# Optimization experiments

Measured on AMD Instinct MI355X. Metric: run time of the kernel, lower is better.

The kernel has to match this reference:

```python
import jax, jax.numpy as jnp
import numpy as np

N = 50000
E = 800000
IN_DIM = 128
HID = 32
HEADS = 4
OUT_DIM = 64
NEG_SLOPE = 0.2


def gat_layer(x, src, dst, W, al, ar, b, heads, dout):
    # x: [N, din]; W: [din, heads*dout]; al/ar: [heads, dout]; b: [heads*dout]
    n = x.shape[0]
    feat = (x @ W).reshape(n, heads, dout)              # [N, H, D]
    el = jnp.sum(feat * al, axis=-1)                    # [N, H] attention (src side)
    er = jnp.sum(feat * ar, axis=-1)                    # [N, H] attention (dst side)
    e = jax.nn.leaky_relu(el[src] + er[dst], NEG_SLOPE)  # [E, H]
    # segment softmax over incoming edges of each destination node
    m = jax.ops.segment_max(e, dst, num_segments=n)     # [N, H]
    ex = jnp.exp(e - m[dst])                            # [E, H]
    s = jax.ops.segment_sum(ex, dst, num_segments=n)    # [N, H]
    alpha = ex / s[dst]                                 # [E, H]
    msg = alpha[:, :, None] * feat[src]                 # [E, H, D]
    out = jax.ops.segment_sum(msg, dst, num_segments=n)  # [N, H, D]
    return out + b.reshape(1, heads, dout)


def setup_inputs() -> dict:
    key = jax.random.key(0)
    ks = jax.random.split(key, 16)
    h = jax.random.normal(ks[0], (N, IN_DIM), dtype=jnp.float32)
    src = jax.random.randint(ks[1], (E,), 0, N, dtype=jnp.int32)
    dst = jax.random.randint(ks[2], (E,), 0, N, dtype=jnp.int32)

    def glorot(k, shape):
        fan = shape[0] + shape[-1]
        return jax.random.normal(k, shape, dtype=jnp.float32) * np.sqrt(2.0 / fan)

    W1 = glorot(ks[3], (IN_DIM, HEADS * HID))
    al1 = glorot(ks[4], (HEADS, HID))
    ar1 = glorot(ks[5], (HEADS, HID))
    b1 = jnp.zeros((HEADS * HID,), dtype=jnp.float32)
    W2 = glorot(ks[6], (HEADS * HID, HEADS * HID))
    al2 = glorot(ks[7], (HEADS, HID))
    ar2 = glorot(ks[8], (HEADS, HID))
    b2 = jnp.zeros((HEADS * HID,), dtype=jnp.float32)
    W3 = glorot(ks[9], (HEADS * HID, OUT_DIM))
    al3 = glorot(ks[10], (1, OUT_DIM))
    ar3 = glorot(ks[11], (1, OUT_DIM))
    b3 = jnp.zeros((OUT_DIM,), dtype=jnp.float32)
    return {"h": h, "src": src, "dst": dst,
            "W1": W1, "al1": al1, "ar1": ar1, "b1": b1,
            "W2": W2, "al2": al2, "ar2": ar2, "b2": b2,
            "W3": W3, "al3": al3, "ar3": ar3, "b3": b3}


def reference(h, src, dst, W1, al1, ar1, b1, W2, al2, ar2, b2, W3, al3, ar3, b3):
    # dropout layers are identity in eval mode
    x = gat_layer(h, src, dst, W1, al1, ar1, b1, HEADS, HID).reshape(N, -1)
    x = jax.nn.elu(x)
    x = gat_layer(x, src, dst, W2, al2, ar2, b2, HEADS, HID).reshape(N, -1)
    x = jax.nn.elu(x)
    x = gat_layer(x, src, dst, W3, al3, ar3, b3, 1, OUT_DIM).mean(axis=1)
    return x
```

## Files before the change

kernel.cpp:

```cpp
#include <hip/hip_runtime.h>
#include <hip/hip_bf16.h>
#include <math.h>

#define NNODES 50000
#define NEDGES 800000

static inline int cdiv(int a, int b) { return (a + b - 1) / b; }


__global__ void zero_deg(int* __restrict__ deg) {
    int i = blockIdx.x * blockDim.x + threadIdx.x;
    if (i < NNODES) deg[i] = 0;
}

__global__ void count_deg(const int* __restrict__ dst, int* __restrict__ deg) {
    int e = blockIdx.x * blockDim.x + threadIdx.x;
    if (e < NEDGES) atomicAdd(&deg[dst[e]], 1);
}

__global__ void scan_rowptr(const int* __restrict__ deg, int* __restrict__ rowptr,
                            int* __restrict__ cursor) {
    __shared__ int wsum[16];
    __shared__ int wpre[16];
    const int tid = threadIdx.x;
    const int lane = tid & 63, wid = tid >> 6;
    int carry = 0;
    const int ntiles = (NNODES + 4095) / 4096;
    for (int t = 0; t < ntiles; t++) {
        int i0 = t * 4096 + tid * 4;
        int4 v = make_int4(0, 0, 0, 0);
        if (i0 < NNODES) v = *(const int4*)&deg[i0];
        int lsum = v.x + v.y + v.z + v.w;
        int x = lsum;
#pragma unroll
        for (int off = 1; off < 64; off <<= 1) {
            int y = __shfl_up(x, off);
            if (lane >= off) x += y;
        }
        if (lane == 63) wsum[wid] = x;
        __syncthreads();
        if (wid == 0) {
            int w = (lane < 16) ? wsum[lane] : 0;
            int xs = w;
#pragma unroll
            for (int off = 1; off < 16; off <<= 1) {
                int y = __shfl_up(xs, off);
                if (lane >= off) xs += y;
            }
            if (lane < 16) wpre[lane] = xs - w;
        }
        __syncthreads();
        int excl = carry + wpre[wid] + x - lsum;
        if (i0 < NNODES) {
            int4 r;
            r.x = excl; r.y = r.x + v.x; r.z = r.y + v.y; r.w = r.z + v.z;
            *(int4*)&rowptr[i0] = r;
            *(int4*)&cursor[i0] = r;
        }
        carry += wpre[15] + wsum[15];
        __syncthreads();
    }
    if (tid == 0) rowptr[NNODES] = carry;
}

__global__ void scatter_src(const int* __restrict__ src, const int* __restrict__ dst,
                            int* __restrict__ cursor, int* __restrict__ csr_src) {
    int e = blockIdx.x * blockDim.x + threadIdx.x;
    if (e < NEDGES) {
        int pos = atomicAdd(&cursor[dst[e]], 1);
        csr_src[pos] = src[e];
    }
}

template <int DIN, int DOUT, int H, int NB>
__global__ void gemm_attn(const float* __restrict__ x, const float* __restrict__ W,
                          const float* __restrict__ al, const float* __restrict__ ar,
                          __hip_bfloat16* __restrict__ feat, float* __restrict__ el,
                          float* __restrict__ er) {
    constexpr int D = DOUT / H;
    __shared__ float xs[NB * DIN];
    const int node0 = blockIdx.x * NB;
    const int d = threadIdx.x;

    const float4* xg = (const float4*)&x[node0 * DIN];
    float4* xs4 = (float4*)xs;
    for (int idx = d; idx < NB * DIN / 4; idx += DOUT) xs4[idx] = xg[idx];
    __syncthreads();

    float accv[NB];
#pragma unroll
    for (int nb = 0; nb < NB; nb++) accv[nb] = 0.f;

    for (int k = 0; k < DIN; k++) {
        float w = W[k * DOUT + d];
#pragma unroll
        for (int nb = 0; nb < NB; nb++) accv[nb] += xs[nb * DIN + k] * w;
    }

    const float alv = al[d], arv = ar[d];
    const int h = d / D;
#pragma unroll
    for (int nb = 0; nb < NB; nb++) {
        float a = accv[nb];
        feat[(node0 + nb) * DOUT + d] = __float2bfloat16(a);
        float pl = a * alv, pr = a * arv;
#pragma unroll
        for (int off = D / 2; off > 0; off >>= 1) {
            pl += __shfl_xor(pl, off);
            pr += __shfl_xor(pr, off);
        }
        if ((d & (D - 1)) == 0) {
            el[(node0 + nb) * H + h] = pl;
            er[(node0 + nb) * H + h] = pr;
        }
    }
}

template <int DOUT, int H>
__global__ void node_aggregate(const int* __restrict__ rowptr, const int* __restrict__ csr_src,
                               const float* __restrict__ el, const float* __restrict__ er,
                               const __hip_bfloat16* __restrict__ feat,
                               const float* __restrict__ b,
                               float* __restrict__ xout, int do_elu) {
    constexpr int D = DOUT / H;
    constexpr int PL = DOUT / 64;
    const int lane = threadIdx.x & 63;
    const int wid = threadIdx.x >> 6;
    const int n = blockIdx.x * (blockDim.x >> 6) + wid;
    if (n >= NNODES) return;
    const int base = rowptr[n];
    const int deg = rowptr[n + 1] - base;

    const int h = (lane * PL) / D;
    const float erh = er[n * H + h];

    float s = 0.f;
    float acc[PL];
#pragma unroll
    for (int p = 0; p < PL; p++) acc[p] = 0.f;

    int j = 0;
    for (; j + 1 < deg; j += 2) {
        int sn0 = csr_src[base + j];
        int sn1 = csr_src[base + j + 1];
        float e0 = el[sn0 * H + h] + erh;
        float e1 = el[sn1 * H + h] + erh;
        e0 = e0 > 0.f ? e0 : 0.2f * e0;
        e1 = e1 > 0.f ? e1 : 0.2f * e1;
        float p0 = __expf(e0);
        float p1 = __expf(e1);
        s += p0 + p1;
        const __hip_bfloat16* f0 = &feat[sn0 * DOUT + lane * PL];
        const __hip_bfloat16* f1 = &feat[sn1 * DOUT + lane * PL];
        if constexpr (PL == 2) {
            float2 a0 = __bfloat1622float2(*(const __hip_bfloat162*)f0);
            float2 a1 = __bfloat1622float2(*(const __hip_bfloat162*)f1);
            acc[0] += p0 * a0.x + p1 * a1.x;
            acc[1] += p0 * a0.y + p1 * a1.y;
        } else {
            acc[0] += p0 * __bfloat162float(f0[0]) + p1 * __bfloat162float(f1[0]);
        }
    }
    if (j < deg) {
        int sn0 = csr_src[base + j];
        float e0 = el[sn0 * H + h] + erh;
        e0 = e0 > 0.f ? e0 : 0.2f * e0;
        float p0 = __expf(e0);
        s += p0;
        const __hip_bfloat16* f0 = &feat[sn0 * DOUT + lane * PL];
        if constexpr (PL == 2) {
            float2 a0 = __bfloat1622float2(*(const __hip_bfloat162*)f0);
            acc[0] += p0 * a0.x;
            acc[1] += p0 * a0.y;
        } else {
            acc[0] += p0 * __bfloat162float(f0[0]);
        }
    }

    float inv = (s > 0.f) ? 1.f / s : 0.f;
#pragma unroll
    for (int p = 0; p < PL; p++) {
        int d = lane * PL + p;
        float v = acc[p] * inv + b[d];
        if (do_elu) v = v > 0.f ? v : expm1f(v);
        xout[n * DOUT + d] = v;
    }
}

extern "C" void kernel_launch(void* const* d_in, const int* in_sizes, int n_in,
                              void* d_out, int out_size, void* d_ws, size_t ws_size,
                              hipStream_t stream) {
    const float* h   = (const float*)d_in[0];
    const int*   src = (const int*)d_in[1];
    const int*   dst = (const int*)d_in[2];
    const float* W1  = (const float*)d_in[3];
    const float* al1 = (const float*)d_in[4];
    const float* ar1 = (const float*)d_in[5];
    const float* b1  = (const float*)d_in[6];
    const float* W2  = (const float*)d_in[7];
    const float* al2 = (const float*)d_in[8];
    const float* ar2 = (const float*)d_in[9];
    const float* b2  = (const float*)d_in[10];
    const float* W3  = (const float*)d_in[11];
    const float* al3 = (const float*)d_in[12];
    const float* ar3 = (const float*)d_in[13];
    const float* b3  = (const float*)d_in[14];

    float* ws = (float*)d_ws;
    __hip_bfloat16* feat = (__hip_bfloat16*)ws;
    float* x2 = ws + NNODES * 64;
    float* x3 = x2 + NNODES * 128;
    float* el = x3 + NNODES * 128;
    float* er = el + NNODES * 4;
    int* deg     = (int*)(er + NNODES * 4);
    int* rowptr  = deg + NNODES;
    int* cursor  = rowptr + NNODES + 4;
    int* csr_src = cursor + NNODES;

    const dim3 B(256);

    zero_deg<<<cdiv(NNODES, 256), B, 0, stream>>>(deg);
    count_deg<<<cdiv(NEDGES, 256), B, 0, stream>>>(dst, deg);
    scan_rowptr<<<1, 1024, 0, stream>>>(deg, rowptr, cursor);
    scatter_src<<<cdiv(NEDGES, 256), B, 0, stream>>>(src, dst, cursor, csr_src);

    gemm_attn<128, 128, 4, 16><<<NNODES / 16, 128, 0, stream>>>(h, W1, al1, ar1, feat, el, er);
    node_aggregate<128, 4><<<cdiv(NNODES, 4), B, 0, stream>>>(rowptr, csr_src, el, er, feat, b1, x2, 1);

    gemm_attn<128, 128, 4, 16><<<NNODES / 16, 128, 0, stream>>>(x2, W2, al2, ar2, feat, el, er);
    node_aggregate<128, 4><<<cdiv(NNODES, 4), B, 0, stream>>>(rowptr, csr_src, el, er, feat, b2, x3, 1);

    gemm_attn<128, 64, 1, 16><<<NNODES / 16, 64, 0, stream>>>(x3, W3, al3, ar3, feat, el, er);
    node_aggregate<64, 1><<<cdiv(NNODES, 4), B, 0, stream>>>(rowptr, csr_src, el, er, feat, b3, (float*)d_out, 0);
}
```

Measured before the change: 497.9 us.

## Register-tile the feature GEMM and batch edge softmax weights per wavefront

The feature GEMM now uses 64-node by full-width shared-memory tiles with K-blocking, and each thread computes a 4x(NT) register tile using float4 LDS reads instead of one column over 16 nodes. The aggregation kernel computes the attention exponentials cooperatively: each lane handles one edge in 64-edge chunks, stores the per-head weights in LDS and broadcasts source indices by shuffle. This removes redundant el gathers and exp work per lane and reduces serial dependency in the edge loop. The cost is extra LDS traffic and a cross-lane reduction for the softmax denominators.

```diff
diff --git a/kernel.cpp b/kernel.cpp
--- a/kernel.cpp
+++ b/kernel.cpp
@@ -72,112 +72,178 @@
     }
 }
 
-template <int DIN, int DOUT, int H, int NB>
-__global__ void gemm_attn(const float* __restrict__ x, const float* __restrict__ W,
-                          const float* __restrict__ al, const float* __restrict__ ar,
-                          __hip_bfloat16* __restrict__ feat, float* __restrict__ el,
-                          float* __restrict__ er) {
+template <int DIN, int DOUT, int H>
+__global__ __launch_bounds__(256) void gemm_attn_rt(
+    const float* __restrict__ x, const float* __restrict__ W,
+    const float* __restrict__ al, const float* __restrict__ ar,
+    __hip_bfloat16* __restrict__ feat, float* __restrict__ el,
+    float* __restrict__ er) {
+    constexpr int BM = 64, BK = 32;
+    constexpr int CG = DOUT / 4;
+    constexpr int NG = 256 / CG;
+    constexpr int NT = BM / NG;
     constexpr int D = DOUT / H;
-    __shared__ float xs[NB * DIN];
-    const int node0 = blockIdx.x * NB;
-    const int d = threadIdx.x;
-
-    const float4* xg = (const float4*)&x[node0 * DIN];
-    float4* xs4 = (float4*)xs;
-    for (int idx = d; idx < NB * DIN / 4; idx += DOUT) xs4[idx] = xg[idx];
-    __syncthreads();
-
-    float accv[NB];
-#pragma unroll
-    for (int nb = 0; nb < NB; nb++) accv[nb] = 0.f;
-
-    for (int k = 0; k < DIN; k++) {
-        float w = W[k * DOUT + d];
-#pragma unroll
-        for (int nb = 0; nb < NB; nb++) accv[nb] += xs[nb * DIN + k] * w;
-    }
-
-    const float alv = al[d], arv = ar[d];
-    const int h = d / D;
-#pragma unroll
-    for (int nb = 0; nb < NB; nb++) {
-        float a = accv[nb];
-        feat[(node0 + nb) * DOUT + d] = __float2bfloat16(a);
-        float pl = a * alv, pr = a * arv;
-#pragma unroll
-        for (int off = D / 2; off > 0; off >>= 1) {
+    constexpr int CPH = D / 4;
+    constexpr int XP = BM + 4;
+
+    __shared__ float xs[BK][XP];
+    __shared__ float ws[BK][DOUT];
+
+    const int t = threadIdx.x;
+    const int node0 = blockIdx.x * BM;
+    const int cg = t % CG, ng = t / CG;
+    const int c0 = cg * 4, n0 = ng * NT;
+
+    float acc[NT][4];
+#pragma unroll
+    for (int i = 0; i < NT; i++)
+#pragma unroll
+        for (int j = 0; j < 4; j++) acc[i][j] = 0.f;
+
+    for (int k0 = 0; k0 < DIN; k0 += BK) {
+        for (int i = t * 4; i < BK * DOUT; i += 256 * 4) {
+            int kk = i / DOUT, c = i % DOUT;
+            *(float4*)&ws[kk][c] = *(const float4*)&W[(k0 + kk) * DOUT + c];
+        }
+        for (int i = t; i < BK * BM; i += 256) {
+            int kk = i & (BK - 1), nd = i >> 5;
+            int node = node0 + nd;
+            xs[kk][nd] = (node < NNODES) ? x[node * DIN + k0 + kk] : 0.f;
+        }
+        __syncthreads();
+        for (int k = 0; k < BK; k++) {
+            const float4 wv = *(const float4*)&ws[k][c0];
+#pragma unroll
+            for (int i0 = 0; i0 < NT; i0 += 4) {
+                const float4 xv = *(const float4*)&xs[k][n0 + i0];
+                acc[i0 + 0][0] += xv.x * wv.x; acc[i0 + 0][1] += xv.x * wv.y;
+                acc[i0 + 0][2] += xv.x * wv.z; acc[i0 + 0][3] += xv.x * wv.w;
+                acc[i0 + 1][0] += xv.y * wv.x; acc[i0 + 1][1] += xv.y * wv.y;
+                acc[i0 + 1][2] += xv.y * wv.z; acc[i0 + 1][3] += xv.y * wv.w;
+                acc[i0 + 2][0] += xv.z * wv.x; acc[i0 + 2][1] += xv.z * wv.y;
+                acc[i0 + 2][2] += xv.z * wv.z; acc[i0 + 2][3] += xv.z * wv.w;
+                acc[i0 + 3][0] += xv.w * wv.x; acc[i0 + 3][1] += xv.w * wv.y;
+                acc[i0 + 3][2] += xv.w * wv.z; acc[i0 + 3][3] += xv.w * wv.w;
+            }
+        }
+        __syncthreads();
+    }
+
+    const float4 alv = *(const float4*)&al[c0];
+    const float4 arv = *(const float4*)&ar[c0];
+    const int head = c0 / D;
+#pragma unroll
+    for (int i = 0; i < NT; i++) {
+        const int node = node0 + n0 + i;
+        float ax = acc[i][0], ay = acc[i][1], az = acc[i][2], aw = acc[i][3];
+        if (node < NNODES) {
+            ushort4 u;
+            u.x = __bfloat16_as_ushort(__float2bfloat16(ax));
+            u.y = __bfloat16_as_ushort(__float2bfloat16(ay));
+            u.z = __bfloat16_as_ushort(__float2bfloat16(az));
+            u.w = __bfloat16_as_ushort(__float2bfloat16(aw));
+            *(ushort4*)&feat[node * DOUT + c0] = u;
+        }
+        float pl = ax * alv.x + ay * alv.y + az * alv.z + aw * alv.w;
+        float pr = ax * arv.x + ay * arv.y + az * arv.z + aw * arv.w;
+#pragma unroll
+        for (int off = CPH / 2; off > 0; off >>= 1) {
             pl += __shfl_xor(pl, off);
             pr += __shfl_xor(pr, off);
         }
-        if ((d & (D - 1)) == 0) {
-            el[(node0 + nb) * H + h] = pl;
-            er[(node0 + nb) * H + h] = pr;
+        if ((cg % CPH) == 0 && node < NNODES) {
+            el[node * H + head] = pl;
+            er[node * H + head] = pr;
         }
     }
 }
 
 template <int DOUT, int H>
-__global__ void node_aggregate(const int* __restrict__ rowptr, const int* __restrict__ csr_src,
-                               const float* __restrict__ el, const float* __restrict__ er,
-                               const __hip_bfloat16* __restrict__ feat,
-                               const float* __restrict__ b,
-                               float* __restrict__ xout, int do_elu) {
+__global__ __launch_bounds__(256) void node_aggregate2(
+    const int* __restrict__ rowptr, const int* __restrict__ csr_src,
+    const float* __restrict__ el, const float* __restrict__ er,
+    const __hip_bfloat16* __restrict__ feat, const float* __restrict__ b,
+    float* __restrict__ xout, int do_elu) {
     constexpr int D = DOUT / H;
     constexpr int PL = DOUT / 64;
+    __shared__ float plds[4][64 * H];
+
     const int lane = threadIdx.x & 63;
     const int wid = threadIdx.x >> 6;
-    const int n = blockIdx.x * (blockDim.x >> 6) + wid;
+    const int n = blockIdx.x * 4 + wid;
     if (n >= NNODES) return;
     const int base = rowptr[n];
     const int deg = rowptr[n + 1] - base;
 
     const int h = (lane * PL) / D;
-    const float erh = er[n * H + h];
-
-    float s = 0.f;
+
+    float erv[H];
+    if constexpr (H == 4) {
+        float4 t = *(const float4*)&er[n * 4];
+        erv[0] = t.x; erv[1] = t.y; erv[2] = t.z; erv[3] = t.w;
+    } else {
+        erv[0] = er[n];
+    }
+
+    float sacc[H];
+#pragma unroll
+    for (int q = 0; q < H; q++) sacc[q] = 0.f;
     float acc[PL];
 #pragma unroll
     for (int p = 0; p < PL; p++) acc[p] = 0.f;
 
-    int j = 0;
-    for (; j + 1 < deg; j += 2) {
-        int sn0 = csr_src[base + j];
-        int sn1 = csr_src[base + j + 1];
-        float e0 = el[sn0 * H + h] + erh;
-        float e1 = el[sn1 * H + h] + erh;
-        e0 = e0 > 0.f ? e0 : 0.2f * e0;
-        e1 = e1 > 0.f ? e1 : 0.2f * e1;
-        float p0 = __expf(e0);
-        float p1 = __expf(e1);
-        s += p0 + p1;
-        const __hip_bfloat16* f0 = &feat[sn0 * DOUT + lane * PL];
-        const __hip_bfloat16* f1 = &feat[sn1 * DOUT + lane * PL];
-        if constexpr (PL == 2) {
-            float2 a0 = __bfloat1622float2(*(const __hip_bfloat162*)f0);
-            float2 a1 = __bfloat1622float2(*(const __hip_bfloat162*)f1);
-            acc[0] += p0 * a0.x + p1 * a1.x;
-            acc[1] += p0 * a0.y + p1 * a1.y;
+    for (int c0 = 0; c0 < deg; c0 += 64) {
+        const int cnt = min(64, deg - c0);
+        int sn = 0;
+        float p4[H];
+#pragma unroll
+        for (int q = 0; q < H; q++) p4[q] = 0.f;
+        if (lane < cnt) {
+            sn = csr_src[base + c0 + lane];
+            if constexpr (H == 4) {
+                float4 t = *(const float4*)&el[sn * 4];
+                float ev[4] = {t.x, t.y, t.z, t.w};
+#pragma unroll
+                for (int q = 0; q < 4; q++) {
+                    float e = ev[q] + erv[q];
+                    e = e > 0.f ? e : 0.2f * e;
+                    p4[q] = __expf(e);
+                    sacc[q] += p4[q];
+                }
+            } else {
+                float e = el[sn] + erv[0];
+                e = e > 0.f ? e : 0.2f * e;
+                p4[0] = __expf(e);
+                sacc[0] += p4[0];
+            }
+        }
+        if constexpr (H == 4) {
+            float4 w = {p4[0], p4[1], p4[2], p4[3]};
+            *(float4*)&plds[wid][lane * 4] = w;
         } else {
-            acc[0] += p0 * __bfloat162float(f0[0]) + p1 * __bfloat162float(f1[0]);
-        }
-    }
-    if (j < deg) {
-        int sn0 = csr_src[base + j];
-        float e0 = el[sn0 * H + h] + erh;
-        e0 = e0 > 0.f ? e0 : 0.2f * e0;
-        float p0 = __expf(e0);
-        s += p0;
-        const __hip_bfloat16* f0 = &feat[sn0 * DOUT + lane * PL];
-        if constexpr (PL == 2) {
-            float2 a0 = __bfloat1622float2(*(const __hip_bfloat162*)f0);
-            acc[0] += p0 * a0.x;
-            acc[1] += p0 * a0.y;
-        } else {
-            acc[0] += p0 * __bfloat162float(f0[0]);
-        }
-    }
-
-    float inv = (s > 0.f) ? 1.f / s : 0.f;
+            plds[wid][lane] = p4[0];
+        }
+        for (int j = 0; j < cnt; j++) {
+            int snj = __shfl(sn, j);
+            float pj = plds[wid][j * H + h];
+            const __hip_bfloat16* f = &feat[snj * DOUT + lane * PL];
+            if constexpr (PL == 2) {
+                float2 a = __bfloat1622float2(*(const __hip_bfloat162*)f);
+                acc[0] += pj * a.x;
+                acc[1] += pj * a.y;
+            } else {
+                acc[0] += pj * __bfloat162float(f[0]);
+            }
+        }
+    }
+
+#pragma unroll
+    for (int off = 32; off > 0; off >>= 1)
+#pragma unroll
+        for (int q = 0; q < H; q++) sacc[q] += __shfl_xor(sacc[q], off);
+    const float s = sacc[h];
+    const float inv = (s > 0.f) ? 1.f / s : 0.f;
+
 #pragma unroll
     for (int p = 0; p < PL; p++) {
         int d = lane * PL + p;
@@ -224,12 +290,12 @@
     scan_rowptr<<<1, 1024, 0, stream>>>(deg, rowptr, cursor);
     scatter_src<<<cdiv(NEDGES, 256), B, 0, stream>>>(src, dst, cursor, csr_src);
 
-    gemm_attn<128, 128, 4, 16><<<NNODES / 16, 128, 0, stream>>>(h, W1, al1, ar1, feat, el, er);
-    node_aggregate<128, 4><<<cdiv(NNODES, 4), B, 0, stream>>>(rowptr, csr_src, el, er, feat, b1, x2, 1);
-
-    gemm_attn<128, 128, 4, 16><<<NNODES / 16, 128, 0, stream>>>(x2, W2, al2, ar2, feat, el, er);
-    node_aggregate<128, 4><<<cdiv(NNODES, 4), B, 0, stream>>>(rowptr, csr_src, el, er, feat, b2, x3, 1);
-
-    gemm_attn<128, 64, 1, 16><<<NNODES / 16, 64, 0, stream>>>(x3, W3, al3, ar3, feat, el, er);
-    node_aggregate<64, 1><<<cdiv(NNODES, 4), B, 0, stream>>>(rowptr, csr_src, el, er, feat, b3, (float*)d_out, 0);
-}
+    gemm_attn_rt<128, 128, 4><<<cdiv(NNODES, 64), B, 0, stream>>>(h, W1, al1, ar1, feat, el, er);
+    node_aggregate2<128, 4><<<cdiv(NNODES, 4), B, 0, stream>>>(rowptr, csr_src, el, er, feat, b1, x2, 1);
+
+    gemm_attn_rt<128, 128, 4><<<cdiv(NNODES, 64), B, 0, stream>>>(x2, W2, al2, ar2, feat, el, er);
+    node_aggregate2<128, 4><<<cdiv(NNODES, 4), B, 0, stream>>>(rowptr, csr_src, el, er, feat, b2, x3, 1);
+
+    gemm_attn_rt<128, 64, 1><<<cdiv(NNODES, 64), B, 0, stream>>>(x3, W3, al3, ar3, feat, el, er);
+    node_aggregate2<64, 1><<<cdiv(NNODES, 4), B, 0, stream>>>(rowptr, csr_src, el, er, feat, b3, (float*)d_out, 0);
+}
```

New measurement: 462.7 us. 1.08x faster.

## Register-tile the projection GEMM and unroll edge aggregation by four

Applied to the files above, without the earlier changes.

Replaces the per-column GEMM, where each thread held one output column for 16 nodes and read W from global memory, with a 128-node by BK=32 shared-memory tiled GEMM. Each thread computes an NT×8 register tile from float4 shared loads, and the attention dot products are reduced across lanes per head. The aggregation kernel unrolls the edge loop from 2 to 4 to expose more independent gathers, and writes outputs as float2. The workspace layout is also recomputed in bytes. The aim is more data reuse in the GEMM and more memory-level parallelism in the gather, at the cost of more registers per thread.

```diff
diff --git a/kernel.cpp b/kernel.cpp
--- a/kernel.cpp
+++ b/kernel.cpp
@@ -72,118 +72,183 @@
     }
 }
 
-template <int DIN, int DOUT, int H, int NB>
-__global__ void gemm_attn(const float* __restrict__ x, const float* __restrict__ W,
-                          const float* __restrict__ al, const float* __restrict__ ar,
-                          __hip_bfloat16* __restrict__ feat, float* __restrict__ el,
-                          float* __restrict__ er) {
+template <int DOUT, int H>
+__global__ __launch_bounds__(256) void gemm_attn_rt2(
+    const float* __restrict__ x, const float* __restrict__ W,
+    const float* __restrict__ al, const float* __restrict__ ar,
+    __hip_bfloat16* __restrict__ feat, float* __restrict__ el,
+    float* __restrict__ er) {
+    constexpr int BM = 128, BK = 32;
+    constexpr int NC = 8;
+    constexpr int CG = DOUT / NC;
+    constexpr int NG = 256 / CG;
+    constexpr int NT = BM / NG;
     constexpr int D = DOUT / H;
-    __shared__ float xs[NB * DIN];
-    const int node0 = blockIdx.x * NB;
-    const int d = threadIdx.x;
-
-    const float4* xg = (const float4*)&x[node0 * DIN];
-    float4* xs4 = (float4*)xs;
-    for (int idx = d; idx < NB * DIN / 4; idx += DOUT) xs4[idx] = xg[idx];
-    __syncthreads();
-
-    float accv[NB];
-#pragma unroll
-    for (int nb = 0; nb < NB; nb++) accv[nb] = 0.f;
-
-    for (int k = 0; k < DIN; k++) {
-        float w = W[k * DOUT + d];
-#pragma unroll
-        for (int nb = 0; nb < NB; nb++) accv[nb] += xs[nb * DIN + k] * w;
-    }
-
-    const float alv = al[d], arv = ar[d];
-    const int h = d / D;
-#pragma unroll
-    for (int nb = 0; nb < NB; nb++) {
-        float a = accv[nb];
-        feat[(node0 + nb) * DOUT + d] = __float2bfloat16(a);
-        float pl = a * alv, pr = a * arv;
-#pragma unroll
-        for (int off = D / 2; off > 0; off >>= 1) {
+    constexpr int CPH = D / NC;
+    constexpr int XP = BM + 4;
+
+    __shared__ float xs[BK][XP];
+    __shared__ float ws[BK][DOUT];
+
+    const int t = threadIdx.x;
+    const int node0 = blockIdx.x * BM;
+    const int cg = t % CG, ng = t / CG;
+    const int c0 = cg * NC, n0 = ng * NT;
+
+    float acc[NT][NC];
+#pragma unroll
+    for (int i = 0; i < NT; i++)
+#pragma unroll
+        for (int j = 0; j < NC; j++) acc[i][j] = 0.f;
+
+    for (int k0 = 0; k0 < 128; k0 += BK) {
+        for (int i = t * 4; i < BK * DOUT; i += 256 * 4) {
+            int kk = i / DOUT, c = i % DOUT;
+            *(float4*)&ws[kk][c] = *(const float4*)&W[(k0 + kk) * DOUT + c];
+        }
+        for (int i = t; i < BK * BM; i += 256) {
+            int kk = i & (BK - 1), nd = i >> 5;
+            int node = node0 + nd;
+            xs[kk][nd] = (node < NNODES) ? x[node * 128 + k0 + kk] : 0.f;
+        }
+        __syncthreads();
+        for (int k = 0; k < BK; k++) {
+            const float4 wa = *(const float4*)&ws[k][c0];
+            const float4 wb = *(const float4*)&ws[k][c0 + 4];
+            float wv[NC] = {wa.x, wa.y, wa.z, wa.w, wb.x, wb.y, wb.z, wb.w};
+#pragma unroll
+            for (int i0 = 0; i0 < NT; i0 += 4) {
+                const float4 xv = *(const float4*)&xs[k][n0 + i0];
+                float xvv[4] = {xv.x, xv.y, xv.z, xv.w};
+#pragma unroll
+                for (int ii = 0; ii < 4; ii++)
+#pragma unroll
+                    for (int q = 0; q < NC; q++)
+                        acc[i0 + ii][q] += xvv[ii] * wv[q];
+            }
+        }
+        __syncthreads();
+    }
+
+    const float4 ala = *(const float4*)&al[c0];
+    const float4 alb = *(const float4*)&al[c0 + 4];
+    const float4 ara = *(const float4*)&ar[c0];
+    const float4 arb = *(const float4*)&ar[c0 + 4];
+    const float alv[NC] = {ala.x, ala.y, ala.z, ala.w, alb.x, alb.y, alb.z, alb.w};
+    const float arv[NC] = {ara.x, ara.y, ara.z, ara.w, arb.x, arb.y, arb.z, arb.w};
+    const int head = c0 / D;
+#pragma unroll
+    for (int i = 0; i < NT; i++) {
+        const int node = node0 + n0 + i;
+        float pl = 0.f, pr = 0.f;
+        if (node < NNODES) {
+            ushort4 u0, u1;
+            u0.x = __bfloat16_as_ushort(__float2bfloat16(acc[i][0]));
+            u0.y = __bfloat16_as_ushort(__float2bfloat16(acc[i][1]));
+            u0.z = __bfloat16_as_ushort(__float2bfloat16(acc[i][2]));
+            u0.w = __bfloat16_as_ushort(__float2bfloat16(acc[i][3]));
+            u1.x = __bfloat16_as_ushort(__float2bfloat16(acc[i][4]));
+            u1.y = __bfloat16_as_ushort(__float2bfloat16(acc[i][5]));
+            u1.z = __bfloat16_as_ushort(__float2bfloat16(acc[i][6]));
+            u1.w = __bfloat16_as_ushort(__float2bfloat16(acc[i][7]));
+            *(ushort4*)&feat[node * DOUT + c0] = u0;
+            *(ushort4*)&feat[node * DOUT + c0 + 4] = u1;
+        }
+#pragma unroll
+        for (int q = 0; q < NC; q++) {
+            pl += acc[i][q] * alv[q];
+            pr += acc[i][q] * arv[q];
+        }
+#pragma unroll
+        for (int off = CPH / 2; off > 0; off >>= 1) {
             pl += __shfl_xor(pl, off);
             pr += __shfl_xor(pr, off);
         }
-        if ((d & (D - 1)) == 0) {
-            el[(node0 + nb) * H + h] = pl;
-            er[(node0 + nb) * H + h] = pr;
+        if ((cg % CPH) == 0 && node < NNODES) {
+            el[node * H + head] = pl;
+            er[node * H + head] = pr;
         }
     }
 }
 
 template <int DOUT, int H>
-__global__ void node_aggregate(const int* __restrict__ rowptr, const int* __restrict__ csr_src,
-                               const float* __restrict__ el, const float* __restrict__ er,
-                               const __hip_bfloat16* __restrict__ feat,
-                               const float* __restrict__ b,
-                               float* __restrict__ xout, int do_elu) {
+__global__ __launch_bounds__(256) void node_aggregate3(
+    const int* __restrict__ rowptr, const int* __restrict__ csr_src,
+    const float* __restrict__ el, const float* __restrict__ er,
+    const __hip_bfloat16* __restrict__ feat, const float* __restrict__ b,
+    float* __restrict__ xout, int do_elu) {
     constexpr int D = DOUT / H;
     constexpr int PL = DOUT / 64;
     const int lane = threadIdx.x & 63;
     const int wid = threadIdx.x >> 6;
-    const int n = blockIdx.x * (blockDim.x >> 6) + wid;
+    const int n = blockIdx.x * 4 + wid;
     if (n >= NNODES) return;
     const int base = rowptr[n];
     const int deg = rowptr[n + 1] - base;
 
     const int h = (lane * PL) / D;
     const float erh = er[n * H + h];
+    const int* cs = &csr_src[base];
 
     float s = 0.f;
-    float acc[PL];
-#pragma unroll
-    for (int p = 0; p < PL; p++) acc[p] = 0.f;
+    float a0 = 0.f, a1 = 0.f;
 
     int j = 0;
-    for (; j + 1 < deg; j += 2) {
-        int sn0 = csr_src[base + j];
-        int sn1 = csr_src[base + j + 1];
+    for (; j + 3 < deg; j += 4) {
+        int sn0 = cs[j], sn1 = cs[j + 1], sn2 = cs[j + 2], sn3 = cs[j + 3];
         float e0 = el[sn0 * H + h] + erh;
         float e1 = el[sn1 * H + h] + erh;
+        float e2 = el[sn2 * H + h] + erh;
+        float e3 = el[sn3 * H + h] + erh;
         e0 = e0 > 0.f ? e0 : 0.2f * e0;
         e1 = e1 > 0.f ? e1 : 0.2f * e1;
-        float p0 = __expf(e0);
-        float p1 = __expf(e1);
-        s += p0 + p1;
-        const __hip_bfloat16* f0 = &feat[sn0 * DOUT + lane * PL];
-        const __hip_bfloat16* f1 = &feat[sn1 * DOUT + lane * PL];
+        e2 = e2 > 0.f ? e2 : 0.2f * e2;
+        e3 = e3 > 0.f ? e3 : 0.2f * e3;
+        float p0 = __expf(e0), p1 = __expf(e1), p2 = __expf(e2), p3 = __expf(e3);
+        s += (p0 + p1) + (p2 + p3);
         if constexpr (PL == 2) {
-            float2 a0 = __bfloat1622float2(*(const __hip_bfloat162*)f0);
-            float2 a1 = __bfloat1622float2(*(const __hip_bfloat162*)f1);
-            acc[0] += p0 * a0.x + p1 * a1.x;
-            acc[1] += p0 * a0.y + p1 * a1.y;
+            float2 f0 = __bfloat1622float2(*(const __hip_bfloat162*)&feat[sn0 * DOUT + lane * 2]);
+            float2 f1 = __bfloat1622float2(*(const __hip_bfloat162*)&feat[sn1 * DOUT + lane * 2]);
+            float2 f2 = __bfloat1622float2(*(const __hip_bfloat162*)&feat[sn2 * DOUT + lane * 2]);
+            float2 f3 = __bfloat1622float2(*(const __hip_bfloat162*)&feat[sn3 * DOUT + lane * 2]);
+            a0 += p0 * f0.x + p1 * f1.x + p2 * f2.x + p3 * f3.x;
+            a1 += p0 * f0.y + p1 * f1.y + p2 * f2.y + p3 * f3.y;
         } else {
-            acc[0] += p0 * __bfloat162float(f0[0]) + p1 * __bfloat162float(f1[0]);
-        }
-    }
-    if (j < deg) {
-        int sn0 = csr_src[base + j];
+            a0 += p0 * __bfloat162float(feat[sn0 * DOUT + lane])
+                + p1 * __bfloat162float(feat[sn1 * DOUT + lane])
+                + p2 * __bfloat162float(feat[sn2 * DOUT + lane])
+                + p3 * __bfloat162float(feat[sn3 * DOUT + lane]);
+        }
+    }
+    for (; j < deg; j++) {
+        int sn0 = cs[j];
         float e0 = el[sn0 * H + h] + erh;
         e0 = e0 > 0.f ? e0 : 0.2f * e0;
         float p0 = __expf(e0);
         s += p0;
-        const __hip_bfloat16* f0 = &feat[sn0 * DOUT + lane * PL];
         if constexpr (PL == 2) {
-            float2 a0 = __bfloat1622float2(*(const __hip_bfloat162*)f0);
-            acc[0] += p0 * a0.x;
-            acc[1] += p0 * a0.y;
+            float2 f0 = __bfloat1622float2(*(const __hip_bfloat162*)&feat[sn0 * DOUT + lane * 2]);
+            a0 += p0 * f0.x;
+            a1 += p0 * f0.y;
         } else {
-            acc[0] += p0 * __bfloat162float(f0[0]);
-        }
-    }
-
-    float inv = (s > 0.f) ? 1.f / s : 0.f;
-#pragma unroll
-    for (int p = 0; p < PL; p++) {
-        int d = lane * PL + p;
-        float v = acc[p] * inv + b[d];
-        if (do_elu) v = v > 0.f ? v : expm1f(v);
-        xout[n * DOUT + d] = v;
+            a0 += p0 * __bfloat162float(feat[sn0 * DOUT + lane]);
+        }
+    }
+
+    const float inv = (s > 0.f) ? 1.f / s : 0.f;
+    if constexpr (PL == 2) {
+        float v0 = a0 * inv + b[lane * 2];
+        float v1 = a1 * inv + b[lane * 2 + 1];
+        if (do_elu) {
+            v0 = v0 > 0.f ? v0 : expm1f(v0);
+            v1 = v1 > 0.f ? v1 : expm1f(v1);
+        }
+        float2 o = {v0, v1};
+        *(float2*)&xout[n * DOUT + lane * 2] = o;
+    } else {
+        float v0 = a0 * inv + b[lane];
+        if (do_elu) v0 = v0 > 0.f ? v0 : expm1f(v0);
+        xout[n * DOUT + lane] = v0;
     }
 }
 
@@ -206,16 +271,16 @@
     const float* ar3 = (const float*)d_in[13];
     const float* b3  = (const float*)d_in[14];
 
-    float* ws = (float*)d_ws;
-    __hip_bfloat16* feat = (__hip_bfloat16*)ws;
-    float* x2 = ws + NNODES * 64;
-    float* x3 = x2 + NNODES * 128;
-    float* el = x3 + NNODES * 128;
-    float* er = el + NNODES * 4;
-    int* deg     = (int*)(er + NNODES * 4);
-    int* rowptr  = deg + NNODES;
-    int* cursor  = rowptr + NNODES + 4;
-    int* csr_src = cursor + NNODES;
+    char* w = (char*)d_ws;
+    __hip_bfloat16* feat = (__hip_bfloat16*)w;  w += (size_t)NNODES * 128 * 2;
+    float* x2 = (float*)w;                      w += (size_t)NNODES * 128 * 4;
+    float* x3 = (float*)w;                      w += (size_t)NNODES * 128 * 4;
+    float* el = (float*)w;                      w += (size_t)NNODES * 4 * 4;
+    float* er = (float*)w;                      w += (size_t)NNODES * 4 * 4;
+    int* deg     = (int*)w;                     w += (size_t)NNODES * 4;
+    int* rowptr  = (int*)w;                     w += (size_t)(NNODES + 4) * 4;
+    int* cursor  = (int*)w;                     w += (size_t)NNODES * 4;
+    int* csr_src = (int*)w;
 
     const dim3 B(256);
 
@@ -224,12 +289,12 @@
     scan_rowptr<<<1, 1024, 0, stream>>>(deg, rowptr, cursor);
     scatter_src<<<cdiv(NEDGES, 256), B, 0, stream>>>(src, dst, cursor, csr_src);
 
-    gemm_attn<128, 128, 4, 16><<<NNODES / 16, 128, 0, stream>>>(h, W1, al1, ar1, feat, el, er);
-    node_aggregate<128, 4><<<cdiv(NNODES, 4), B, 0, stream>>>(rowptr, csr_src, el, er, feat, b1, x2, 1);
-
-    gemm_attn<128, 128, 4, 16><<<NNODES / 16, 128, 0, stream>>>(x2, W2, al2, ar2, feat, el, er);
-    node_aggregate<128, 4><<<cdiv(NNODES, 4), B, 0, stream>>>(rowptr, csr_src, el, er, feat, b2, x3, 1);
-
-    gemm_attn<128, 64, 1, 16><<<NNODES / 16, 64, 0, stream>>>(x3, W3, al3, ar3, feat, el, er);
-    node_aggregate<64, 1><<<cdiv(NNODES, 4), B, 0, stream>>>(rowptr, csr_src, el, er, feat, b3, (float*)d_out, 0);
-}
+    gemm_attn_rt2<128, 4><<<cdiv(NNODES, 128), B, 0, stream>>>(h, W1, al1, ar1, feat, el, er);
+    node_aggregate3<128, 4><<<cdiv(NNODES, 4), B, 0, stream>>>(rowptr, csr_src, el, er, feat, b1, x2, 1);
+
+    gemm_attn_rt2<128, 4><<<cdiv(NNODES, 128), B, 0, stream>>>(x2, W2, al2, ar2, feat, el, er);
+    node_aggregate3<128, 4><<<cdiv(NNODES, 4), B, 0, stream>>>(rowptr, csr_src, el, er, feat, b2, x3, 1);
+
+    gemm_attn_rt2<64, 1><<<cdiv(NNODES, 128), B, 0, stream>>>(x3, W3, al3, ar3, feat, el, er);
+    node_aggregate3<64, 1><<<cdiv(NNODES, 4), B, 0, stream>>>(rowptr, csr_src, el, er, feat, b3, (float*)d_out, 0);
+}
```

Measured after the change: 432.8 us. 13.1% less time.
